# Optimization experiments

Hardware: AMD Instinct MI355X
Metric: run time of the kernel (lower is better)

## Reference

```python
import jax, jax.numpy as jnp
import numpy as np

B, N, K, H, W = 8, 64, 32, 256, 256


def setup_inputs() -> dict:
    key = jax.random.key(0)
    k1, k2, k3, k4, k5, k6 = jax.random.split(key, 6)
    original = jax.random.normal(k1, (B, 3, H, W), dtype=jnp.float32)
    # loc = (cx, cy, w, h) in normalized coords; keep w,h >= 0.05 so the
    # unnormalized gaussian stays finite.
    cxy = jax.random.uniform(k2, (B, N, 2), dtype=jnp.float32)
    wh = jax.random.uniform(k3, (B, N, 2), dtype=jnp.float32) * 0.45 + 0.05
    loc = jnp.concatenate([cxy, wh], axis=-1)
    masks = jax.random.normal(k4, (B, N, K), dtype=jnp.float32)
    proto = jax.random.normal(k5, (B, H, W, K), dtype=jnp.float32)
    conf = jax.random.uniform(k6, (B, N), dtype=jnp.float32)
    return {"original": original, "loc": loc, "masks": masks,
            "proto": proto, "conf": conf}


def _unnormal_gaussian(loc, h, w):
    # Unnormalized 2D axis-aligned gaussian per prior, evaluated on a
    # half-pixel normalized grid. loc: [B, N, 4] = (cx, cy, sx, sy).
    ys = (jnp.arange(h, dtype=loc.dtype) + 0.5) / h  # [H]
    xs = (jnp.arange(w, dtype=loc.dtype) + 0.5) / w  # [W]
    cx = loc[..., 0][:, :, None, None]
    cy = loc[..., 1][:, :, None, None]
    sx = loc[..., 2][:, :, None, None]
    sy = loc[..., 3][:, :, None, None]
    dy = (ys[None, None, :, None] - cy) / sy  # [B,N,H,1]
    dx = (xs[None, None, None, :] - cx) / sx  # [B,N,1,W]
    return jnp.exp(-0.5 * (dx * dx + dy * dy))  # [B,N,H,W]


def reference(original, loc, masks, proto, conf):
    b, c, h, w = original.shape
    gauss = _unnormal_gaussian(loc, h, w)  # [B,N,H,W]
    # lincomb: sigmoid(proto @ mask_coeffs^T) -> assembled instance masks
    assembled = jax.nn.sigmoid(jnp.einsum('bhwk,bnk->bnhw', proto, masks))
    attention = assembled * gauss                      # [B,N,H,W]
    mask_conf = attention * conf[:, :, None, None]     # einsum 'abcd,ab->abcd'
    denom = jnp.sum(mask_conf, axis=1, keepdims=True) + 1e-5
    final_conf = 1.0 - jnp.sum(mask_conf * mask_conf / denom, axis=1)  # [B,H,W]
    # F.interpolate(..., resizeShape, 'bilinear'): proto res == resizeShape,
    # so this is an identity bilinear resize (half-pixel convention).
    resized_conf = jax.image.resize(final_conf, (b, h, w), method='bilinear')
    total_conf = jnp.sum(resized_conf, axis=0)                        # [H,W]
    weighted_mean = jnp.einsum('bchw,bhw->chw', original, resized_conf)
    squared_diff = (original - weighted_mean) ** 2                    # [B,C,H,W]
    weighted_diff = squared_diff * resized_conf[:, None]  # 'abcd,acd->abcd'
    weighted_variance = weighted_diff / total_conf
    return jnp.sum(weighted_variance)
```

## Files before the change

kernel.cpp:

```cpp
#include <hip/hip_runtime.h>
#include <hip/hip_bf16.h>

#define NPIX 65536
#define NB 8
#define NN 64
#define KK 32
#define LOG2E 1.4426950408889634f

typedef __attribute__((ext_vector_type(4))) float f32x4;
typedef __attribute__((ext_vector_type(8))) short bf16x8;

__device__ __forceinline__ float rcpf(float x) { return __builtin_amdgcn_rcpf(x); }
__device__ __forceinline__ float exp2_fast(float x) { float r; asm("v_exp_f32 %0, %1" : "=v"(r) : "v"(x)); return r; }
__device__ __forceinline__ float log2_fast(float x) { float r; asm("v_log_f32 %0, %1" : "=v"(r) : "v"(x)); return r; }
__device__ __forceinline__ short f2bf(float x) {
    union { __hip_bfloat16 b; short s; } u; u.b = __float2bfloat16(x); return u.s;
}

__global__ __launch_bounds__(256) void k_phase1(
    const float* __restrict__ loc,
    const float* __restrict__ masks,
    const float* __restrict__ proto,
    const float* __restrict__ conf,
    float* __restrict__ fcb)
{
    __shared__ float4 sprm[NN];

    const int b    = blockIdx.x >> 8;
    const int row  = blockIdx.x & 255;
    const int tid  = threadIdx.x;
    const int lane = tid & 63;
    const int wave = tid >> 6;
    const int nl   = lane & 15;
    const int kg   = lane >> 4;

    const float inv = 1.0f / 256.0f;

    float4 mu0[4], mu1[4];
#pragma unroll
    for (int t = 0; t < 4; ++t) {
        const float* mp = masks + ((size_t)b * NN + 16 * t + nl) * KK + kg * 8;
        mu0[t] = *(const float4*)mp;
        mu1[t] = *(const float4*)(mp + 4);
    }

    if (tid < NN) {
        float4 L = ((const float4*)loc)[b * NN + tid];
        float isx = rcpf(L.z), isy = rcpf(L.w);
        float gx = -0.72134752f * isx * isx;
        float gy = -0.72134752f * isy * isy;
        float fyr = (row + 0.5f) * inv;
        float dy  = fyr - L.y;
        float ey  = fmaf(dy * dy, gy, log2_fast(conf[b * NN + tid]));
        float beta  = -2.0f * gx * L.x;
        float gamma = fmaf(gx * L.x, L.x, ey);
        sprm[tid] = make_float4(gx, beta, gamma, 0.f);
    }
    __syncthreads();

    int mi[4], ni0;
    {
        bf16x8 Ap, Bp;
#pragma unroll
        for (int j = 0; j < 8; ++j) { Ap[j] = 0; Bp[j] = 0; }
        if (kg == 0) {
            Ap[0] = f2bf((float)nl);
            Ap[1] = f2bf(1.0f);
            Bp[0] = f2bf(1.0f);
            Bp[1] = f2bf((float)(16 * nl));
        }
        f32x4 z = {0.f, 0.f, 0.f, 0.f};
        f32x4 d = __builtin_amdgcn_mfma_f32_16x16x32_bf16(Ap, Bp, z, 0, 0, 0);
#pragma unroll
        for (int r = 0; r < 4; ++r) {
            int v = (int)(d[r] + 0.5f);
            mi[r] = v & 15;
            if (r == 0) ni0 = (v >> 4) & 15;
        }
    }

    bf16x8 Mf[4];
#pragma unroll
    for (int t = 0; t < 4; ++t) {
        bf16x8 v;
        v[0] = f2bf(mu0[t].x * -LOG2E); v[1] = f2bf(mu0[t].y * -LOG2E);
        v[2] = f2bf(mu0[t].z * -LOG2E); v[3] = f2bf(mu0[t].w * -LOG2E);
        v[4] = f2bf(mu1[t].x * -LOG2E); v[5] = f2bf(mu1[t].y * -LOG2E);
        v[6] = f2bf(mu1[t].z * -LOG2E); v[7] = f2bf(mu1[t].w * -LOG2E);
        Mf[t] = v;
    }

    float Pa[4][4], Pb[4][4], Pc[4][4];
#pragma unroll
    for (int t = 0; t < 4; ++t)
#pragma unroll
        for (int r = 0; r < 4; ++r) {
            float4 P = sprm[16 * t + mi[r]];
            Pa[t][r] = P.x; Pb[t][r] = P.y; Pc[t][r] = P.z;
        }

#define EVALT(ACC, T)                                                       \
    {                                                                       \
        _Pragma("unroll") for (int r = 0; r < 4; ++r) {                     \
            float e  = fmaf(fmaf(Pa[T][r], fx, Pb[T][r]), fx, Pc[T][r]);    \
            float aa = exp2_fast(e) * rcpf(1.0f + exp2_fast(ACC[r]));       \
            S1 += aa; S2 = fmaf(aa, aa, S2);                                \
        }                                                                   \
    }

    const size_t prow = (size_t)b * NPIX + (size_t)row * 256;
    const int pxb = wave * 64;
    const float* pp0 = proto + (prow + pxb + nl) * KK + kg * 8;

    float S1a[4], S2a[4];

    float4 c0 = *(const float4*)(pp0);
    float4 c1 = *(const float4*)(pp0 + 4);

#pragma unroll
    for (int i = 0; i < 4; ++i) {
        float4 n0, n1;
        if (i < 3) {
            const float* np = pp0 + (size_t)(i + 1) * 16 * KK;
            n0 = *(const float4*)np;
            n1 = *(const float4*)(np + 4);
        }

        bf16x8 Pf;
        Pf[0] = f2bf(c0.x); Pf[1] = f2bf(c0.y); Pf[2] = f2bf(c0.z); Pf[3] = f2bf(c0.w);
        Pf[4] = f2bf(c1.x); Pf[5] = f2bf(c1.y); Pf[6] = f2bf(c1.z); Pf[7] = f2bf(c1.w);

        f32x4 z = {0.f, 0.f, 0.f, 0.f};
        f32x4 acc0 = __builtin_amdgcn_mfma_f32_16x16x32_bf16(Mf[0], Pf, z, 0, 0, 0);
        f32x4 acc1 = __builtin_amdgcn_mfma_f32_16x16x32_bf16(Mf[1], Pf, z, 0, 0, 0);
        f32x4 acc2 = __builtin_amdgcn_mfma_f32_16x16x32_bf16(Mf[2], Pf, z, 0, 0, 0);
        f32x4 acc3 = __builtin_amdgcn_mfma_f32_16x16x32_bf16(Mf[3], Pf, z, 0, 0, 0);

        const float fx = (pxb + i * 16 + ni0 + 0.5f) * inv;
        float S1 = 0.f, S2 = 0.f;
        EVALT(acc0, 0);
        EVALT(acc1, 1);
        EVALT(acc2, 2);
        EVALT(acc3, 3);
        S1a[i] = S1; S2a[i] = S2;

        if (i < 3) { c0 = n0; c1 = n1; }
    }
#undef EVALT

#pragma unroll
    for (int i = 0; i < 4; ++i) {
        S1a[i] += __shfl_xor(S1a[i], 16);
        S2a[i] += __shfl_xor(S2a[i], 16);
    }
#pragma unroll
    for (int i = 0; i < 4; ++i) {
        S1a[i] += __shfl_xor(S1a[i], 32);
        S2a[i] += __shfl_xor(S2a[i], 32);
    }
    if (lane < 16) {
#pragma unroll
        for (int i = 0; i < 4; ++i)
            fcb[prow + pxb + i * 16 + ni0] = 1.0f - S2a[i] * rcpf(S1a[i] + 1e-5f);
    }
}

__global__ __launch_bounds__(256) void k_phase2(
    const float* __restrict__ original,
    const float* __restrict__ fcb,
    float* __restrict__ out)
{
    const int pix = blockIdx.x * 256 + threadIdx.x;

    float f[NB];
    float tot = 0.f;
#pragma unroll
    for (int b = 0; b < NB; ++b) { f[b] = fcb[(size_t)b * NPIX + pix]; tot += f[b]; }

    float part = 0.f;
#pragma unroll
    for (int c = 0; c < 3; ++c) {
        float o[NB];
        float wm = 0.f;
#pragma unroll
        for (int b = 0; b < NB; ++b) {
            o[b] = original[((size_t)(b * 3 + c)) * NPIX + pix];
            wm = fmaf(o[b], f[b], wm);
        }
#pragma unroll
        for (int b = 0; b < NB; ++b) {
            float d = o[b] - wm;
            part = fmaf(d * d, f[b], part);
        }
    }
    part *= rcpf(tot);

#pragma unroll
    for (int off = 32; off > 0; off >>= 1) part += __shfl_down(part, off);
    __shared__ float sred[4];
    if ((threadIdx.x & 63) == 0) sred[threadIdx.x >> 6] = part;
    __syncthreads();
    if (threadIdx.x == 0) atomicAdd(out, sred[0] + sred[1] + sred[2] + sred[3]);
}

__global__ __launch_bounds__(256) void k_fused(
    const float* __restrict__ original, const float* __restrict__ loc,
    const float* __restrict__ masks, const float* __restrict__ proto,
    const float* __restrict__ conf, float* __restrict__ out)
{
    const int pix = blockIdx.x * 256 + threadIdx.x;
    const float inv = 1.0f / 256.0f;
    const float fx = ((pix & 255) + 0.5f) * inv;
    const float fy = ((pix >> 8) + 0.5f) * inv;

    float f[NB];
    for (int b = 0; b < NB; ++b) {
        const float4* p4 = (const float4*)(proto + ((size_t)b * NPIX + pix) * KK);
        const float4* m4 = (const float4*)(masks + (size_t)b * NN * KK);
        const float4* l4 = (const float4*)(loc + (size_t)b * NN * 4);
        const float*  cf = conf + b * NN;
        float S1 = 0.f, S2 = 0.f;
        for (int n = 0; n < NN; ++n) {
            float sa = 0.f;
#pragma unroll
            for (int j = 0; j < 8; ++j) {
                float4 A = p4[j], m = m4[n * 8 + j];
                sa = fmaf(A.w, m.w, fmaf(A.z, m.z, fmaf(A.y, m.y, fmaf(A.x, m.x, sa))));
            }
            const float4 L = l4[n];
            float isx = rcpf(L.z), isy = rcpf(L.w);
            float dx = (fx - L.x) * isx, dy = (fy - L.y) * isy;
            float g = __expf(-0.5f * fmaf(dx, dx, dy * dy));
            float a = g * rcpf(1.0f + __expf(-sa)) * cf[n];
            S1 += a;
            S2 = fmaf(a, a, S2);
        }
        f[b] = 1.0f - S2 * rcpf(S1 + 1e-5f);
    }
    float tot = 0.f;
#pragma unroll
    for (int b = 0; b < NB; ++b) tot += f[b];
    float part = 0.f;
#pragma unroll
    for (int c = 0; c < 3; ++c) {
        float o[NB];
        float wm = 0.f;
#pragma unroll
        for (int b = 0; b < NB; ++b) {
            o[b] = original[((size_t)(b * 3 + c)) * NPIX + pix];
            wm = fmaf(o[b], f[b], wm);
        }
#pragma unroll
        for (int b = 0; b < NB; ++b) {
            float d = o[b] - wm;
            part = fmaf(d * d, f[b], part);
        }
    }
    part *= rcpf(tot);

#pragma unroll
    for (int off = 32; off > 0; off >>= 1) part += __shfl_down(part, off);
    __shared__ float sred[4];
    if ((threadIdx.x & 63) == 0) sred[threadIdx.x >> 6] = part;
    __syncthreads();
    if (threadIdx.x == 0) atomicAdd(out, sred[0] + sred[1] + sred[2] + sred[3]);
}

extern "C" void kernel_launch(void* const* d_in, const int* in_sizes, int n_in,
                              void* d_out, int out_size, void* d_ws, size_t ws_size,
                              hipStream_t stream) {
    const float* original = (const float*)d_in[0];
    const float* loc      = (const float*)d_in[1];
    const float* masks    = (const float*)d_in[2];
    const float* proto    = (const float*)d_in[3];
    const float* conf     = (const float*)d_in[4];
    float* out = (float*)d_out;

    hipMemsetAsync(out, 0, sizeof(float), stream);

    const size_t fc_bytes = (size_t)NB * NPIX * sizeof(float);
    if (ws_size >= fc_bytes) {
        float* fcb = (float*)d_ws;
        k_phase1<<<NB * 256, 256, 0, stream>>>(loc, masks, proto, conf, fcb);
        k_phase2<<<NPIX / 256, 256, 0, stream>>>(original, fcb, out);
    } else {
        k_fused<<<NPIX / 256, 256, 0, stream>>>(original, loc, masks, proto, conf, out);
    }
}
```

Before: 37.98 us.

## Process two rows per block with 128-pixel waves and deeper proto prefetch

Each phase-1 block now covers two image rows instead of one, with each wave handling 128 pixels (8 chunks) rather than 64. The per-block setup work (mask loads, bf16 conversion, parameter table) is spread over twice the pixels, and the grid is halved. Proto loads are double-buffered two chunks ahead, and the S1/S2 sums are split into four independent accumulators to shorten dependency chains. In exchange each thread holds more registers, which may lower occupancy, and the smaller grid gives fewer blocks to spread across CUs.

```diff
diff --git a/kernel.cpp b/kernel.cpp
--- a/kernel.cpp
+++ b/kernel.cpp
@@ -24,15 +24,18 @@
     const float* __restrict__ conf,
     float* __restrict__ fcb)
 {
-    __shared__ float4 sprm[NN];
-
-    const int b    = blockIdx.x >> 8;
-    const int row  = blockIdx.x & 255;
+    __shared__ float4 sprm[2][NN];
+
+    const int b    = blockIdx.x >> 7;
+    const int rp   = blockIdx.x & 127;
     const int tid  = threadIdx.x;
     const int lane = tid & 63;
     const int wave = tid >> 6;
     const int nl   = lane & 15;
     const int kg   = lane >> 4;
+    const int rw   = wave >> 1;
+    const int half = wave & 1;
+    const int row  = rp * 2 + rw;
 
     const float inv = 1.0f / 256.0f;
 
@@ -44,17 +47,18 @@
         mu1[t] = *(const float4*)(mp + 4);
     }
 
-    if (tid < NN) {
-        float4 L = ((const float4*)loc)[b * NN + tid];
+    if (tid < 128) {
+        const int rr = tid >> 6, n = tid & 63;
+        float4 L = ((const float4*)loc)[b * NN + n];
         float isx = rcpf(L.z), isy = rcpf(L.w);
         float gx = -0.72134752f * isx * isx;
         float gy = -0.72134752f * isy * isy;
-        float fyr = (row + 0.5f) * inv;
+        float fyr = (rp * 2 + rr + 0.5f) * inv;
         float dy  = fyr - L.y;
-        float ey  = fmaf(dy * dy, gy, log2_fast(conf[b * NN + tid]));
+        float ey  = fmaf(dy * dy, gy, log2_fast(conf[b * NN + n]));
         float beta  = -2.0f * gx * L.x;
         float gamma = fmaf(gx * L.x, L.x, ey);
-        sprm[tid] = make_float4(gx, beta, gamma, 0.f);
+        sprm[rr][n] = make_float4(gx, beta, gamma, 0.f);
     }
     __syncthreads();
 
@@ -95,7 +99,7 @@
     for (int t = 0; t < 4; ++t)
 #pragma unroll
         for (int r = 0; r < 4; ++r) {
-            float4 P = sprm[16 * t + mi[r]];
+            float4 P = sprm[rw][16 * t + mi[r]];
             Pa[t][r] = P.x; Pb[t][r] = P.y; Pc[t][r] = P.z;
         }
 
@@ -104,31 +108,36 @@
         _Pragma("unroll") for (int r = 0; r < 4; ++r) {                     \
             float e  = fmaf(fmaf(Pa[T][r], fx, Pb[T][r]), fx, Pc[T][r]);    \
             float aa = exp2_fast(e) * rcpf(1.0f + exp2_fast(ACC[r]));       \
-            S1 += aa; S2 = fmaf(aa, aa, S2);                                \
+            s1[T] += aa; s2[T] = fmaf(aa, aa, s2[T]);                       \
         }                                                                   \
     }
 
     const size_t prow = (size_t)b * NPIX + (size_t)row * 256;
-    const int pxb = wave * 64;
+    const int pxb = half * 128;
     const float* pp0 = proto + (prow + pxb + nl) * KK + kg * 8;
 
-    float S1a[4], S2a[4];
-
-    float4 c0 = *(const float4*)(pp0);
-    float4 c1 = *(const float4*)(pp0 + 4);
-
-#pragma unroll
-    for (int i = 0; i < 4; ++i) {
+    float4 c0a = *(const float4*)(pp0);
+    float4 c1a = *(const float4*)(pp0 + 4);
+    float4 c0b = *(const float4*)(pp0 + 512);
+    float4 c1b = *(const float4*)(pp0 + 512 + 4);
+
+    float S1a[8], S2a[8];
+
+#pragma unroll
+    for (int i = 0; i < 8; ++i) {
+        float4 cc0 = (i & 1) ? c0b : c0a;
+        float4 cc1 = (i & 1) ? c1b : c1a;
+
         float4 n0, n1;
-        if (i < 3) {
-            const float* np = pp0 + (size_t)(i + 1) * 16 * KK;
+        if (i < 6) {
+            const float* np = pp0 + (size_t)(i + 2) * 512;
             n0 = *(const float4*)np;
             n1 = *(const float4*)(np + 4);
         }
 
         bf16x8 Pf;
-        Pf[0] = f2bf(c0.x); Pf[1] = f2bf(c0.y); Pf[2] = f2bf(c0.z); Pf[3] = f2bf(c0.w);
-        Pf[4] = f2bf(c1.x); Pf[5] = f2bf(c1.y); Pf[6] = f2bf(c1.z); Pf[7] = f2bf(c1.w);
+        Pf[0] = f2bf(cc0.x); Pf[1] = f2bf(cc0.y); Pf[2] = f2bf(cc0.z); Pf[3] = f2bf(cc0.w);
+        Pf[4] = f2bf(cc1.x); Pf[5] = f2bf(cc1.y); Pf[6] = f2bf(cc1.z); Pf[7] = f2bf(cc1.w);
 
         f32x4 z = {0.f, 0.f, 0.f, 0.f};
         f32x4 acc0 = __builtin_amdgcn_mfma_f32_16x16x32_bf16(Mf[0], Pf, z, 0, 0, 0);
@@ -137,30 +146,35 @@
         f32x4 acc3 = __builtin_amdgcn_mfma_f32_16x16x32_bf16(Mf[3], Pf, z, 0, 0, 0);
 
         const float fx = (pxb + i * 16 + ni0 + 0.5f) * inv;
-        float S1 = 0.f, S2 = 0.f;
+        float s1[4] = {0.f, 0.f, 0.f, 0.f};
+        float s2[4] = {0.f, 0.f, 0.f, 0.f};
         EVALT(acc0, 0);
         EVALT(acc1, 1);
         EVALT(acc2, 2);
         EVALT(acc3, 3);
-        S1a[i] = S1; S2a[i] = S2;
-
-        if (i < 3) { c0 = n0; c1 = n1; }
+        S1a[i] = (s1[0] + s1[1]) + (s1[2] + s1[3]);
+        S2a[i] = (s2[0] + s2[1]) + (s2[2] + s2[3]);
+
+        if (i < 6) {
+            if (i & 1) { c0b = n0; c1b = n1; }
+            else       { c0a = n0; c1a = n1; }
+        }
     }
 #undef EVALT
 
 #pragma unroll
-    for (int i = 0; i < 4; ++i) {
+    for (int i = 0; i < 8; ++i) {
         S1a[i] += __shfl_xor(S1a[i], 16);
         S2a[i] += __shfl_xor(S2a[i], 16);
     }
 #pragma unroll
-    for (int i = 0; i < 4; ++i) {
+    for (int i = 0; i < 8; ++i) {
         S1a[i] += __shfl_xor(S1a[i], 32);
         S2a[i] += __shfl_xor(S2a[i], 32);
     }
     if (lane < 16) {
 #pragma unroll
-        for (int i = 0; i < 4; ++i)
+        for (int i = 0; i < 8; ++i)
             fcb[prow + pxb + i * 16 + ni0] = 1.0f - S2a[i] * rcpf(S1a[i] + 1e-5f);
     }
 }
@@ -281,7 +295,7 @@
     const size_t fc_bytes = (size_t)NB * NPIX * sizeof(float);
     if (ws_size >= fc_bytes) {
         float* fcb = (float*)d_ws;
-        k_phase1<<<NB * 256, 256, 0, stream>>>(loc, masks, proto, conf, fcb);
+        k_phase1<<<NB * 128, 256, 0, stream>>>(loc, masks, proto, conf, fcb);
         k_phase2<<<NPIX / 256, 256, 0, stream>>>(original, fcb, out);
     } else {
         k_fused<<<NPIX / 256, 256, 0, stream>>>(original, loc, masks, proto, conf, out);
```

Result: faster. 35.97 us (-5.3%).
